# Kernel optimization log

Hardware: AMD Instinct MI355X
Metric: run time of the kernel (lower is better)

## Reference

```python
import jax, jax.numpy as jnp
import numpy as np

jax.config.update("jax_enable_x64", True)  # hash math needs int64 (prime * coord > 2^31)

LEVEL = 16
MOD_T = 2 ** 16
FDIM = 3
_PRIMES = (1, 2654435761, 805459861)  # first feature_dim primes from the module


def _grid_sizes():
    # mirrors torch float32 computation: b = exp((log(n_max)-log(n_min))/(level-1))
    n_min = np.float32(4.0)
    n_max = np.float32(256.0)
    b = np.float32(np.exp((np.log(n_max) - np.log(n_min)) / np.float32(LEVEL - 1)))
    return [int(n_min * b ** i) for i in range(LEVEL)]


def setup_inputs() -> dict:
    key = jax.random.key(0)
    k1, k2 = jax.random.split(key)
    images = jax.random.uniform(k1, (16, 3, 256, 256), dtype=jnp.float32)
    hash_table = (jax.random.uniform(k2, (LEVEL, MOD_T, FDIM), dtype=jnp.float32)
                  * 0.0002 - 0.0001)
    return {"images": images, "hash_table": hash_table}


def reference(images, hash_table):
    b, c, h, w = images.shape
    primes = jnp.array(_PRIMES[:FDIM], dtype=jnp.int64)
    neg_inf = jnp.array(-jnp.inf, dtype=images.dtype)
    outs = []
    for lvl, grid in enumerate(_grid_sizes()):
        kh, kw = h // grid, w // grid
        # max_pool2d(images*grid, kernel=(kh,kw), stride=(kh,kw))
        pooled = jax.lax.reduce_window(
            images * grid, neg_inf, jax.lax.max,
            window_dimensions=(1, 1, kh, kw),
            window_strides=(1, 1, kh, kw),
            padding="VALID")                     # [B, F, gh, gw]
        idx = pooled.astype(jnp.int64) * primes[None, :, None, None]
        g = idx[:, 0]
        for i in range(1, FDIM):
            g = g ^ idx[:, i]
        g = g % MOD_T                             # [B, gh, gw]
        f = hash_table[lvl][g]                    # gather -> [B, gh, gw, F]
        f = jnp.transpose(f, (0, 3, 1, 2))        # [B, F, gh, gw]
        # F.interpolate(..., mode='bilinear') == half-pixel, align_corners=False
        f = jax.image.resize(f, (b, FDIM, h, w), method="bilinear")
        outs.append(f)
    return jnp.concatenate(outs, axis=1)          # [B, level*F, H, W]
```

## Files before the change

kernel.cpp:

```cpp
#include <hip/hip_runtime.h>
#include <stdint.h>
#include <math.h>


#define NLVL 16
#define NB   16

typedef float nvec4 __attribute__((ext_vector_type(4)));

__constant__ int   c_P[NLVL]   = {4,5,6,9,12,15,21,28,36,51,64,85,128,256,256,256};
__constant__ float c_G[NLVL]   = {4.f,5.f,6.f,9.f,12.f,15.f,21.f,27.f,36.f,48.f,63.f,84.f,111.f,147.f,194.f,255.f};
__constant__ int   c_CUM[14]   = {0,16,41,77,158,302,527,968,1752,3048,5649,9745,16970,33354};

#define CELLS_PB   33354
#define CELLS_TOT  (CELLS_PB*NB)
#define MWS_FLOATS (CELLS_TOT*3)
#define POOL_BLOCKS (NB*64)
#define DIR_BLOCKS  1024
#define TILE_BLOCKS (13*16*16)
#define K2_BLOCKS   (DIR_BLOCKS + TILE_BLOCKS)

__device__ __forceinline__ uint32_t hash3(float m0, float m1, float m2, float g) {
    uint32_t v0 = (uint32_t)(int)(m0 * g);
    uint32_t v1 = (uint32_t)(int)(m1 * g);
    uint32_t v2 = (uint32_t)(int)(m2 * g);
    return (v0 ^ (v1 * 2654435761u) ^ (v2 * 805459861u)) & 0xFFFFu;
}

__device__ __forceinline__ void nt_store4(float* p, float a, float b, float c, float d) {
    nvec4 v; v.x = a; v.y = b; v.z = c; v.w = d;
    __builtin_nontemporal_store(v, (nvec4*)p);
}

__global__ __launch_bounds__(256) void pool_single(const float* __restrict__ img,
                                                   unsigned int* __restrict__ mws)
{
    static constexpr int K_P[13]   = {4,5,6,9,12,15,21,28,36,51,64,85,128};
    static constexpr int K_KH[13]  = {64,51,42,28,21,17,12,9,7,5,4,3,2};
    static constexpr int K_CUM[13] = {0,16,41,77,158,302,527,968,1752,3048,5649,9745,16970};

    __shared__ float simg[3][4][256];
    __shared__ float cmax[3][256];

    int b    = blockIdx.x >> 6;
    int band = blockIdx.x & 63;
    int y0   = band * 4;

    const float* base = img + (size_t)b * 196608 + (size_t)y0 * 256;
    for (int t = threadIdx.x; t < 768; t += 256) {
        int ch  = t >> 8;
        int rem = t & 255;
        int row = rem >> 6, cg = rem & 63;
        float4 v = *(const float4*)(base + (size_t)ch * 65536 + row * 256 + cg * 4);
        int c4 = cg << 2;
        simg[ch][row][c4 + 0] = v.x;
        simg[ch][row][c4 + 1] = v.y;
        simg[ch][row][c4 + 2] = v.z;
        simg[ch][row][c4 + 3] = v.w;
    }
    __syncthreads();

    {
        int x = threadIdx.x;
#pragma unroll
        for (int ch = 0; ch < 3; ++ch)
            cmax[ch][x] = fmaxf(fmaxf(simg[ch][0][x], simg[ch][1][x]),
                                fmaxf(simg[ch][2][x], simg[ch][3][x]));
    }
    __syncthreads();

#pragma unroll
    for (int lvl = 0; lvl < 13; ++lvl) {
        const int kh = K_KH[lvl], P = K_P[lvl];
        int nr0 = y0 / kh;
        int nr1 = (y0 + 3) / kh; if (nr1 > P - 1) nr1 = P - 1;
        int cnt = (nr1 - nr0 + 1) * P;
        for (int t = threadIdx.x; t < cnt; t += 256) {
            int dcr = t / P;
            int cx  = t - dcr * P;
            int cr  = nr0 + dcr;
            int rlo = cr * kh;      if (rlo < y0) rlo = y0;
            int rhi = cr * kh + kh; if (rhi > y0 + 4) rhi = y0 + 4;
            int cA = cx * kh, cB = cA + kh;
            float m0 = -INFINITY, m1 = -INFINITY, m2 = -INFINITY;
            if (rlo == y0 && rhi == y0 + 4) {
                for (int c = cA; c < cB; ++c) {
                    m0 = fmaxf(m0, cmax[0][c]);
                    m1 = fmaxf(m1, cmax[1][c]);
                    m2 = fmaxf(m2, cmax[2][c]);
                }
            } else {
                for (int r = rlo; r < rhi; ++r) {
                    int rr = r - y0;
                    for (int c = cA; c < cB; ++c) {
                        m0 = fmaxf(m0, simg[0][rr][c]);
                        m1 = fmaxf(m1, simg[1][rr][c]);
                        m2 = fmaxf(m2, simg[2][rr][c]);
                    }
                }
            }
            int idx = K_CUM[lvl] * NB + b * P * P + cr * P + cx;
            if (kh == 2 || kh == 4) {
                mws[idx]                 = __float_as_uint(m0);
                mws[idx + CELLS_TOT]     = __float_as_uint(m1);
                mws[idx + 2 * CELLS_TOT] = __float_as_uint(m2);
            } else {
                atomicMax(&mws[idx],                 __float_as_uint(m0));
                atomicMax(&mws[idx + CELLS_TOT],     __float_as_uint(m1));
                atomicMax(&mws[idx + 2 * CELLS_TOT], __float_as_uint(m2));
            }
        }
    }
}

__global__ __launch_bounds__(256) void render(const float* __restrict__ img,
                                              const float* __restrict__ tab,
                                              const float* __restrict__ mws,
                                              float* __restrict__ out)
{
    __shared__ float4 s[34 * 34];
    if (blockIdx.x < DIR_BLOCKS) {
        int t = blockIdx.x * 256 + threadIdx.x;
        int b = t >> 14;
        int pix0 = (t & 16383) << 2;
        const float* p = img + (size_t)b * 196608 + pix0;
        float4 i0 = *(const float4*)p;
        float4 i1 = *(const float4*)(p + 65536);
        float4 i2 = *(const float4*)(p + 131072);
#pragma unroll
        for (int lvl = 13; lvl < 16; ++lvl) {
            float g = c_G[lvl];
            const float* T = tab + (size_t)lvl * 196608;
            uint32_t g0 = hash3(i0.x, i1.x, i2.x, g);
            uint32_t g1 = hash3(i0.y, i1.y, i2.y, g);
            uint32_t g2 = hash3(i0.z, i1.z, i2.z, g);
            uint32_t g3 = hash3(i0.w, i1.w, i2.w, g);
            float3 f0 = *(const float3*)(T + g0 * 3);
            float3 f1 = *(const float3*)(T + g1 * 3);
            float3 f2 = *(const float3*)(T + g2 * 3);
            float3 f3 = *(const float3*)(T + g3 * 3);
            float* ob = out + ((size_t)b * 48 + 3 * lvl) * 65536 + pix0;
            nt_store4(ob,            f0.x, f1.x, f2.x, f3.x);
            nt_store4(ob + 65536,    f0.y, f1.y, f2.y, f3.y);
            nt_store4(ob + 131072,   f0.z, f1.z, f2.z, f3.z);
        }
        return;
    }

    int blk   = blockIdx.x - DIR_BLOCKS;
    int tile  = blk & 15;
    int plane = blk >> 4;
    int lvl   = plane >> 4;
    int b     = plane & 15;
    int P     = c_P[lvl];
    int yt0   = (tile >> 2) * 64;
    int xt0   = (tile & 3) * 64;

    int nlo  = ((2 * yt0 + 1) * P - 256) >> 9;
    int r_lo = nlo < 0 ? 0 : (nlo > P - 1 ? P - 1 : nlo);
    int nhi  = (((2 * (yt0 + 63) + 1) * P - 256) >> 9) + 1;
    int r_hi = nhi < 0 ? 0 : (nhi > P - 1 ? P - 1 : nhi);
    int mlo  = ((2 * xt0 + 1) * P - 256) >> 9;
    int c_lo = mlo < 0 ? 0 : (mlo > P - 1 ? P - 1 : mlo);
    int mhi  = (((2 * (xt0 + 63) + 1) * P - 256) >> 9) + 1;
    int c_hi = mhi < 0 ? 0 : (mhi > P - 1 ? P - 1 : mhi);
    int span_y = r_hi - r_lo + 1;
    int span_x = c_hi - c_lo + 1;

    int planebase = c_CUM[lvl] * NB + b * P * P;
    const float* T = tab + (size_t)lvl * 196608;
    float gmul = c_G[lvl];
    int n = span_y * span_x;
    for (int t = threadIdx.x; t < n; t += 256) {
        int r = t / span_x, c = t - r * span_x;
        int idx = planebase + (r_lo + r) * P + c_lo + c;
        float m0 = mws[idx];
        float m1 = mws[idx + CELLS_TOT];
        float m2 = mws[idx + 2 * CELLS_TOT];
        uint32_t g = hash3(m0, m1, m2, gmul);
        float3 tv = *(const float3*)(T + g * 3);
        float4 fv; fv.x = tv.x; fv.y = tv.y; fv.z = tv.z; fv.w = 0.f;
        s[t] = fv;
    }
    __syncthreads();

    int lane = threadIdx.x & 63;
    int w    = threadIdx.x >> 6;
    int x    = xt0 + lane;

    int numx = (2 * x + 1) * P - 256;
    int ix0  = numx >> 9;
    float fx = (float)(numx & 511) * (1.0f / 512.0f);
    int ix1;
    if (ix0 < 0)           { ix0 = 0;     ix1 = 0;     fx = 0.f; }
    else if (ix0 >= P - 1) { ix0 = P - 1; ix1 = P - 1; fx = 0.f; }
    else                   { ix1 = ix0 + 1; }
    int cA = ix0 - c_lo, cB = ix1 - c_lo;
    float wx0 = 1.f - fx, wx1 = fx;

    int cur0 = -1, cur1 = -1;
    float r0x = 0.f, r0y = 0.f, r0z = 0.f;
    float r1x = 0.f, r1y = 0.f, r1z = 0.f;
    float* obase = out + ((size_t)b * 48 + 3 * lvl) * 65536 + x;

    for (int k = 0; k < 16; ++k) {
        int y = yt0 + w * 16 + k;
        int numy = (2 * y + 1) * P - 256;
        int iy0  = numy >> 9;
        float fy = (float)(numy & 511) * (1.0f / 512.0f);
        int iy1;
        if (iy0 < 0)           { iy0 = 0;     iy1 = 0;     fy = 0.f; }
        else if (iy0 >= P - 1) { iy0 = P - 1; iy1 = P - 1; fy = 0.f; }
        else                   { iy1 = iy0 + 1; }

        if (iy0 != cur0) {
            if (iy0 == cur1) { r0x = r1x; r0y = r1y; r0z = r1z; }
            else {
                const float4* p = s + (iy0 - r_lo) * span_x;
                float4 a = p[cA], q = p[cB];
                r0x = wx0 * a.x + wx1 * q.x;
                r0y = wx0 * a.y + wx1 * q.y;
                r0z = wx0 * a.z + wx1 * q.z;
            }
            cur0 = iy0;
        }
        if (iy1 != cur1) {
            const float4* p = s + (iy1 - r_lo) * span_x;
            float4 a = p[cA], q = p[cB];
            r1x = wx0 * a.x + wx1 * q.x;
            r1y = wx0 * a.y + wx1 * q.y;
            r1z = wx0 * a.z + wx1 * q.z;
            cur1 = iy1;
        }

        float wy0 = 1.f - fy, wy1 = fy;
        float* o = obase + (size_t)y * 256;
        __builtin_nontemporal_store(wy0 * r0x + wy1 * r1x, o);
        __builtin_nontemporal_store(wy0 * r0y + wy1 * r1y, o + 65536);
        __builtin_nontemporal_store(wy0 * r0z + wy1 * r1z, o + 131072);
    }
}

extern "C" void kernel_launch(void* const* d_in, const int* in_sizes, int n_in,
                              void* d_out, int out_size, void* d_ws, size_t ws_size,
                              hipStream_t stream)
{
    const float* img = (const float*)d_in[0];
    const float* tab = (const float*)d_in[1];
    float* out = (float*)d_out;
    float* mws = (float*)d_ws;

    (void)hipMemsetAsync(mws, 0, (size_t)MWS_FLOATS * sizeof(float), stream);
    hipLaunchKernelGGL(pool_single, dim3(POOL_BLOCKS), dim3(256), 0, stream, img, (unsigned int*)mws);
    hipLaunchKernelGGL(render,      dim3(K2_BLOCKS), dim3(256), 0, stream, img, tab, mws, out);
}
```

Before: 89.73 us.

## Vectorize bilinear tile output to float4 stores and drop nontemporal hints

The tiled upsampling path now has each thread produce a 4-wide strip of x pixels over 4 rows and write float4 stores, where before each thread wrote scalar stores down 16 rows. The per-row reuse of interpolated rows is removed, so every output point does four LDS reads. Output stores in both the direct and tiled paths also switch from nontemporal to regular stores. Wider stores cut the number of store instructions, at the cost of more LDS traffic, and output writes may now pollute the cache.

```diff
diff --git a/kernel.cpp b/kernel.cpp
--- a/kernel.cpp
+++ b/kernel.cpp
@@ -5,8 +5,6 @@
 
 #define NLVL 16
 #define NB   16
-
-typedef float nvec4 __attribute__((ext_vector_type(4)));
 
 __constant__ int   c_P[NLVL]   = {4,5,6,9,12,15,21,28,36,51,64,85,128,256,256,256};
 __constant__ float c_G[NLVL]   = {4.f,5.f,6.f,9.f,12.f,15.f,21.f,27.f,36.f,48.f,63.f,84.f,111.f,147.f,194.f,255.f};
@@ -25,11 +23,6 @@
     uint32_t v1 = (uint32_t)(int)(m1 * g);
     uint32_t v2 = (uint32_t)(int)(m2 * g);
     return (v0 ^ (v1 * 2654435761u) ^ (v2 * 805459861u)) & 0xFFFFu;
-}
-
-__device__ __forceinline__ void nt_store4(float* p, float a, float b, float c, float d) {
-    nvec4 v; v.x = a; v.y = b; v.z = c; v.w = d;
-    __builtin_nontemporal_store(v, (nvec4*)p);
 }
 
 __global__ __launch_bounds__(256) void pool_single(const float* __restrict__ img,
@@ -139,10 +132,15 @@
             float3 f1 = *(const float3*)(T + g1 * 3);
             float3 f2 = *(const float3*)(T + g2 * 3);
             float3 f3 = *(const float3*)(T + g3 * 3);
+            float4 o0, o1, o2;
+            o0.x = f0.x; o1.x = f0.y; o2.x = f0.z;
+            o0.y = f1.x; o1.y = f1.y; o2.y = f1.z;
+            o0.z = f2.x; o1.z = f2.y; o2.z = f2.z;
+            o0.w = f3.x; o1.w = f3.y; o2.w = f3.z;
             float* ob = out + ((size_t)b * 48 + 3 * lvl) * 65536 + pix0;
-            nt_store4(ob,            f0.x, f1.x, f2.x, f3.x);
-            nt_store4(ob + 65536,    f0.y, f1.y, f2.y, f3.y);
-            nt_store4(ob + 131072,   f0.z, f1.z, f2.z, f3.z);
+            *(float4*)ob            = o0;
+            *(float4*)(ob + 65536)  = o1;
+            *(float4*)(ob + 131072) = o2;
         }
         return;
     }
@@ -186,25 +184,26 @@
 
     int lane = threadIdx.x & 63;
     int w    = threadIdx.x >> 6;
-    int x    = xt0 + lane;
-
-    int numx = (2 * x + 1) * P - 256;
-    int ix0  = numx >> 9;
-    float fx = (float)(numx & 511) * (1.0f / 512.0f);
-    int ix1;
-    if (ix0 < 0)           { ix0 = 0;     ix1 = 0;     fx = 0.f; }
-    else if (ix0 >= P - 1) { ix0 = P - 1; ix1 = P - 1; fx = 0.f; }
-    else                   { ix1 = ix0 + 1; }
-    int cA = ix0 - c_lo, cB = ix1 - c_lo;
-    float wx0 = 1.f - fx, wx1 = fx;
-
-    int cur0 = -1, cur1 = -1;
-    float r0x = 0.f, r0y = 0.f, r0z = 0.f;
-    float r1x = 0.f, r1y = 0.f, r1z = 0.f;
-    float* obase = out + ((size_t)b * 48 + 3 * lvl) * 65536 + x;
-
-    for (int k = 0; k < 16; ++k) {
-        int y = yt0 + w * 16 + k;
+    int xq   = lane & 15;
+    int rg   = lane >> 4;
+    int xb   = xt0 + xq * 4;
+
+    int ix0t[4], ix1t[4]; float wx1t[4];
+#pragma unroll
+    for (int j = 0; j < 4; ++j) {
+        int numx = (2 * (xb + j) + 1) * P - 256;
+        int ix0  = numx >> 9;
+        float fx = (float)(numx & 511) * (1.0f / 512.0f);
+        int ix1;
+        if (ix0 < 0)           { ix0 = 0;     ix1 = 0;     fx = 0.f; }
+        else if (ix0 >= P - 1) { ix0 = P - 1; ix1 = P - 1; fx = 0.f; }
+        else                   { ix1 = ix0 + 1; }
+        ix0t[j] = ix0 - c_lo; ix1t[j] = ix1 - c_lo; wx1t[j] = fx;
+    }
+
+#pragma unroll
+    for (int k = 0; k < 4; ++k) {
+        int y = yt0 + w * 16 + rg * 4 + k;
         int numy = (2 * y + 1) * P - 256;
         int iy0  = numy >> 9;
         float fy = (float)(numy & 511) * (1.0f / 512.0f);
@@ -212,32 +211,28 @@
         if (iy0 < 0)           { iy0 = 0;     iy1 = 0;     fy = 0.f; }
         else if (iy0 >= P - 1) { iy0 = P - 1; iy1 = P - 1; fy = 0.f; }
         else                   { iy1 = iy0 + 1; }
-
-        if (iy0 != cur0) {
-            if (iy0 == cur1) { r0x = r1x; r0y = r1y; r0z = r1z; }
-            else {
-                const float4* p = s + (iy0 - r_lo) * span_x;
-                float4 a = p[cA], q = p[cB];
-                r0x = wx0 * a.x + wx1 * q.x;
-                r0y = wx0 * a.y + wx1 * q.y;
-                r0z = wx0 * a.z + wx1 * q.z;
-            }
-            cur0 = iy0;
-        }
-        if (iy1 != cur1) {
-            const float4* p = s + (iy1 - r_lo) * span_x;
-            float4 a = p[cA], q = p[cB];
-            r1x = wx0 * a.x + wx1 * q.x;
-            r1y = wx0 * a.y + wx1 * q.y;
-            r1z = wx0 * a.z + wx1 * q.z;
-            cur1 = iy1;
-        }
-
-        float wy0 = 1.f - fy, wy1 = fy;
-        float* o = obase + (size_t)y * 256;
-        __builtin_nontemporal_store(wy0 * r0x + wy1 * r1x, o);
-        __builtin_nontemporal_store(wy0 * r0y + wy1 * r1y, o + 65536);
-        __builtin_nontemporal_store(wy0 * r0z + wy1 * r1z, o + 131072);
+        const float4* p0 = s + (iy0 - r_lo) * span_x;
+        const float4* p1 = s + (iy1 - r_lo) * span_x;
+        float wy1 = fy, wy0 = 1.f - fy;
+
+        float v[3][4];
+#pragma unroll
+        for (int j = 0; j < 4; ++j) {
+            float wx1 = wx1t[j], wx0 = 1.f - wx1;
+            float4 t00 = p0[ix0t[j]];
+            float4 t01 = p0[ix1t[j]];
+            float4 t10 = p1[ix0t[j]];
+            float4 t11 = p1[ix1t[j]];
+            v[0][j] = wy0 * (wx0 * t00.x + wx1 * t01.x) + wy1 * (wx0 * t10.x + wx1 * t11.x);
+            v[1][j] = wy0 * (wx0 * t00.y + wx1 * t01.y) + wy1 * (wx0 * t10.y + wx1 * t11.y);
+            v[2][j] = wy0 * (wx0 * t00.z + wx1 * t01.z) + wy1 * (wx0 * t10.z + wx1 * t11.z);
+        }
+        float* o = out + ((size_t)b * 48 + 3 * lvl) * 65536 + (size_t)y * 256 + xb;
+#pragma unroll
+        for (int c = 0; c < 3; ++c) {
+            float4 q; q.x = v[c][0]; q.y = v[c][1]; q.z = v[c][2]; q.w = v[c][3];
+            *(float4*)(o + (size_t)c * 65536) = q;
+        }
     }
 }
 
```

Result: no change. 88.04 us (-1.9%).
